# Kernel optimization log

Measured on AMD Instinct MI355X. Metric: run time of the kernel, lower is better.

Reference implementation:

```python
import jax, jax.numpy as jnp
import numpy as np

RANK = 4
IN_FEATURES = 1024
OUT_FEATURES = 1024
ALPHA = 1.0
SCALING = ALPHA / RANK


def setup_inputs() -> dict:
    key = jax.random.key(0)
    kx, ka = jax.random.split(key)
    x = jax.random.normal(kx, (4, 8192, IN_FEATURES), dtype=jnp.float32)
    # kaiming_uniform_(a=sqrt(5)) on [rank, in_features]: bound = sqrt(3) * gain / sqrt(fan_in)
    # gain = sqrt(2/(1+a^2)) = sqrt(1/3); fan_in = in_features -> bound = 1/sqrt(in_features)
    bound = 1.0 / np.sqrt(IN_FEATURES)
    lora_A = jax.random.uniform(ka, (RANK, IN_FEATURES), dtype=jnp.float32, minval=-bound, maxval=bound)
    # original init is zeros for B; use random values so the output/gradients are non-trivial
    lora_B = jax.random.normal(jax.random.fold_in(key, 7), (OUT_FEATURES, RANK), dtype=jnp.float32) * 0.02
    return {"x": x, "lora_A": lora_A, "lora_B": lora_B}


def reference(x, lora_A, lora_B):
    # h = scaling * (x @ A^T) @ B^T   (dropout p=0 -> identity)
    h = jnp.einsum('bsi,ri->bsr', x, lora_A)      # [B, S, rank]
    h = jnp.einsum('bsr,or->bso', h, lora_B)      # [B, S, out_features]
    return h * SCALING
```

## Files before the change

kernel.cpp:

```cpp
#include <hip/hip_runtime.h>
#include <stdint.h>

#define IN_F 1024
#define OUT_F 1024
#define SCALING 0.25f
#define TILE_ROWS 16
#define BLOCK 256

__global__ __launch_bounds__(BLOCK, 3) void lora_tile(
    const float* __restrict__ x, const float* __restrict__ A,
    const float* __restrict__ B, float* __restrict__ out, int nrows) {
  __shared__ float4 hf[TILE_ROWS];

  const int t = threadIdx.x;
  const int lane = t & 63;
  const int wave = t >> 6;
  const int row0 = blockIdx.x * TILE_ROWS;
  if (row0 >= nrows) return;

  const float4* __restrict__ x4 =
      (const float4*)(x + (size_t)(row0 + wave * 4) * IN_F);
  const float4* __restrict__ A4 = (const float4*)A;

  float4 xr[4][4];
#pragma unroll
  for (int i = 0; i < 4; ++i)
#pragma unroll
    for (int k = 0; k < 4; ++k) xr[i][k] = x4[i * 256 + lane + 64 * k];

  float4 a[4][4];
#pragma unroll
  for (int k = 0; k < 4; ++k)
#pragma unroll
    for (int r = 0; r < 4; ++r) a[r][k] = A4[r * 256 + lane + 64 * k];

  float p[4][4];
#pragma unroll
  for (int i = 0; i < 4; ++i)
#pragma unroll
    for (int r = 0; r < 4; ++r) p[i][r] = 0.f;

#pragma unroll
  for (int i = 0; i < 4; ++i)
#pragma unroll
    for (int k = 0; k < 4; ++k) {
      const float4 xv = xr[i][k];
#pragma unroll
      for (int r = 0; r < 4; ++r)
        p[i][r] += xv.x * a[r][k].x + xv.y * a[r][k].y + xv.z * a[r][k].z +
                   xv.w * a[r][k].w;
    }

  const float4* __restrict__ B4 = (const float4*)B;
  const float4 bf0 = B4[4 * t + 0];
  const float4 bf1 = B4[4 * t + 1];
  const float4 bf2 = B4[4 * t + 2];
  const float4 bf3 = B4[4 * t + 3];

#pragma unroll
  for (int off = 1; off < 64; off <<= 1)
#pragma unroll
    for (int i = 0; i < 4; ++i)
#pragma unroll
      for (int r = 0; r < 4; ++r) p[i][r] += __shfl_xor(p[i][r], off, 64);

  if (lane == 0) {
#pragma unroll
    for (int i = 0; i < 4; ++i)
      hf[wave * 4 + i] =
          make_float4(p[i][0] * SCALING, p[i][1] * SCALING, p[i][2] * SCALING,
                      p[i][3] * SCALING);
  }
  __syncthreads();

  float4* __restrict__ out4 = (float4*)out;
#pragma unroll
  for (int r = 0; r < TILE_ROWS; ++r) {
    const float4 h = hf[r];
    float4 res;
    res.x = h.x * bf0.x + h.y * bf0.y + h.z * bf0.z + h.w * bf0.w;
    res.y = h.x * bf1.x + h.y * bf1.y + h.z * bf1.z + h.w * bf1.w;
    res.z = h.x * bf2.x + h.y * bf2.y + h.z * bf2.z + h.w * bf2.w;
    res.w = h.x * bf3.x + h.y * bf3.y + h.z * bf3.z + h.w * bf3.w;
    out4[(size_t)(row0 + r) * (OUT_F / 4) + t] = res;
  }
}

extern "C" void kernel_launch(void* const* d_in, const int* in_sizes, int n_in,
                              void* d_out, int out_size, void* d_ws,
                              size_t ws_size, hipStream_t stream) {
  const float* x = (const float*)d_in[0];
  const float* A = (const float*)d_in[1];
  const float* B = (const float*)d_in[2];
  float* out = (float*)d_out;

  const int nrows = in_sizes[0] / IN_F;
  const int blocks = (nrows + TILE_ROWS - 1) / TILE_ROWS;
  lora_tile<<<blocks, BLOCK, 0, stream>>>(x, A, B, out, nrows);
}
```

Measured before the change: 232.7 us.

## Use persistent waves with register-resident A/B and double-buffered row streaming

Replaces the one-block-per-16-rows grid with a fixed persistent grid of 512 blocks. Each wave loops over 16-row groups, keeping A and B in registers and double-buffering x loads two rows at a time so the next loads overlap the current compute and stores. Each wave handles its own rows end to end, with no shared memory or block barrier. This cuts per-block launch and reload overhead and the sync, but raises register pressure (occupancy hint lowered to 2) and serialises each wave's rows.

```diff
diff --git a/kernel.cpp b/kernel.cpp
--- a/kernel.cpp
+++ b/kernel.cpp
@@ -4,85 +4,134 @@
 #define IN_F 1024
 #define OUT_F 1024
 #define SCALING 0.25f
-#define TILE_ROWS 16
 #define BLOCK 256
+#define NBLOCKS 512
+#define NITER 8
 
-__global__ __launch_bounds__(BLOCK, 3) void lora_tile(
+__global__ __launch_bounds__(BLOCK, 2) void lora_stream(
     const float* __restrict__ x, const float* __restrict__ A,
     const float* __restrict__ B, float* __restrict__ out, int nrows) {
-  __shared__ float4 hf[TILE_ROWS];
+  const int lane = threadIdx.x & 63;
+  const int gwave = (int)((blockIdx.x * BLOCK + threadIdx.x) >> 6);
+  const int nwaves = (int)(gridDim.x * (BLOCK / 64));
 
-  const int t = threadIdx.x;
-  const int lane = t & 63;
-  const int wave = t >> 6;
-  const int row0 = blockIdx.x * TILE_ROWS;
-  if (row0 >= nrows) return;
-
-  const float4* __restrict__ x4 =
-      (const float4*)(x + (size_t)(row0 + wave * 4) * IN_F);
   const float4* __restrict__ A4 = (const float4*)A;
-
-  float4 xr[4][4];
-#pragma unroll
-  for (int i = 0; i < 4; ++i)
-#pragma unroll
-    for (int k = 0; k < 4; ++k) xr[i][k] = x4[i * 256 + lane + 64 * k];
+  const float4* __restrict__ B4 = (const float4*)B;
+  const float4* __restrict__ X4 = (const float4*)x;
+  float4* __restrict__ out4 = (float4*)out;
 
   float4 a[4][4];
 #pragma unroll
+  for (int r = 0; r < 4; ++r)
+#pragma unroll
+    for (int k = 0; k < 4; ++k) a[r][k] = A4[r * 256 + lane + 64 * k];
+
+  float4 b[4][4];
+#pragma unroll
   for (int k = 0; k < 4; ++k)
 #pragma unroll
-    for (int r = 0; r < 4; ++r) a[r][k] = A4[r * 256 + lane + 64 * k];
+    for (int c = 0; c < 4; ++c) b[k][c] = B4[4 * (lane + 64 * k) + c];
 
-  float p[4][4];
+  for (int grp = gwave; grp * 16 < nrows; grp += nwaves) {
+    const int base = grp * 16;
+    if (base + 16 <= nrows) {
+      float4 xr[2][8];
 #pragma unroll
-  for (int i = 0; i < 4; ++i)
+      for (int j = 0; j < 2; ++j)
 #pragma unroll
-    for (int r = 0; r < 4; ++r) p[i][r] = 0.f;
+        for (int k = 0; k < 4; ++k)
+          xr[0][j * 4 + k] = X4[(size_t)(base + j) * 256 + lane + 64 * k];
 
 #pragma unroll
-  for (int i = 0; i < 4; ++i)
+      for (int it = 0; it < NITER; ++it) {
+        if (it + 1 < NITER) {
 #pragma unroll
-    for (int k = 0; k < 4; ++k) {
-      const float4 xv = xr[i][k];
+          for (int j = 0; j < 2; ++j)
 #pragma unroll
-      for (int r = 0; r < 4; ++r)
-        p[i][r] += xv.x * a[r][k].x + xv.y * a[r][k].y + xv.z * a[r][k].z +
-                   xv.w * a[r][k].w;
-    }
+            for (int k = 0; k < 4; ++k)
+              xr[(it + 1) & 1][j * 4 + k] =
+                  X4[(size_t)(base + 2 * (it + 1) + j) * 256 + lane + 64 * k];
+        }
 
-  const float4* __restrict__ B4 = (const float4*)B;
-  const float4 bf0 = B4[4 * t + 0];
-  const float4 bf1 = B4[4 * t + 1];
-  const float4 bf2 = B4[4 * t + 2];
-  const float4 bf3 = B4[4 * t + 3];
+        float p[2][4];
+#pragma unroll
+        for (int j = 0; j < 2; ++j)
+#pragma unroll
+          for (int r = 0; r < 4; ++r) p[j][r] = 0.f;
 
 #pragma unroll
-  for (int off = 1; off < 64; off <<= 1)
+        for (int j = 0; j < 2; ++j)
 #pragma unroll
-    for (int i = 0; i < 4; ++i)
+          for (int k = 0; k < 4; ++k) {
+            const float4 xv = xr[it & 1][j * 4 + k];
 #pragma unroll
-      for (int r = 0; r < 4; ++r) p[i][r] += __shfl_xor(p[i][r], off, 64);
+            for (int r = 0; r < 4; ++r)
+              p[j][r] += xv.x * a[r][k].x + xv.y * a[r][k].y +
+                         xv.z * a[r][k].z + xv.w * a[r][k].w;
+          }
 
-  if (lane == 0) {
 #pragma unroll
-    for (int i = 0; i < 4; ++i)
-      hf[wave * 4 + i] =
-          make_float4(p[i][0] * SCALING, p[i][1] * SCALING, p[i][2] * SCALING,
-                      p[i][3] * SCALING);
-  }
-  __syncthreads();
+        for (int off = 1; off < 64; off <<= 1)
+#pragma unroll
+          for (int j = 0; j < 2; ++j)
+#pragma unroll
+            for (int r = 0; r < 4; ++r)
+              p[j][r] += __shfl_xor(p[j][r], off, 64);
 
-  float4* __restrict__ out4 = (float4*)out;
 #pragma unroll
-  for (int r = 0; r < TILE_ROWS; ++r) {
-    const float4 h = hf[r];
-    float4 res;
-    res.x = h.x * bf0.x + h.y * bf0.y + h.z * bf0.z + h.w * bf0.w;
-    res.y = h.x * bf1.x + h.y * bf1.y + h.z * bf1.z + h.w * bf1.w;
-    res.z = h.x * bf2.x + h.y * bf2.y + h.z * bf2.z + h.w * bf2.w;
-    res.w = h.x * bf3.x + h.y * bf3.y + h.z * bf3.z + h.w * bf3.w;
-    out4[(size_t)(row0 + r) * (OUT_F / 4) + t] = res;
+        for (int j = 0; j < 2; ++j) {
+          const float h0 = p[j][0] * SCALING;
+          const float h1 = p[j][1] * SCALING;
+          const float h2 = p[j][2] * SCALING;
+          const float h3 = p[j][3] * SCALING;
+          const size_t orow = (size_t)(base + 2 * it + j) * 256;
+#pragma unroll
+          for (int k = 0; k < 4; ++k) {
+            float4 res;
+            res.x = h0 * b[k][0].x + h1 * b[k][0].y + h2 * b[k][0].z +
+                    h3 * b[k][0].w;
+            res.y = h0 * b[k][1].x + h1 * b[k][1].y + h2 * b[k][1].z +
+                    h3 * b[k][1].w;
+            res.z = h0 * b[k][2].x + h1 * b[k][2].y + h2 * b[k][2].z +
+                    h3 * b[k][2].w;
+            res.w = h0 * b[k][3].x + h1 * b[k][3].y + h2 * b[k][3].z +
+                    h3 * b[k][3].w;
+            out4[orow + lane + 64 * k] = res;
+          }
+        }
+      }
+    } else {
+      for (int row = base; row < nrows; ++row) {
+        float q[4] = {0.f, 0.f, 0.f, 0.f};
+#pragma unroll
+        for (int k = 0; k < 4; ++k) {
+          const float4 xv = X4[(size_t)row * 256 + lane + 64 * k];
+#pragma unroll
+          for (int r = 0; r < 4; ++r)
+            q[r] += xv.x * a[r][k].x + xv.y * a[r][k].y + xv.z * a[r][k].z +
+                    xv.w * a[r][k].w;
+        }
+#pragma unroll
+        for (int off = 1; off < 64; off <<= 1)
+#pragma unroll
+          for (int r = 0; r < 4; ++r) q[r] += __shfl_xor(q[r], off, 64);
+        const float h0 = q[0] * SCALING, h1 = q[1] * SCALING,
+                    h2 = q[2] * SCALING, h3 = q[3] * SCALING;
+#pragma unroll
+        for (int k = 0; k < 4; ++k) {
+          float4 res;
+          res.x = h0 * b[k][0].x + h1 * b[k][0].y + h2 * b[k][0].z +
+                  h3 * b[k][0].w;
+          res.y = h0 * b[k][1].x + h1 * b[k][1].y + h2 * b[k][1].z +
+                  h3 * b[k][1].w;
+          res.z = h0 * b[k][2].x + h1 * b[k][2].y + h2 * b[k][2].z +
+                  h3 * b[k][2].w;
+          res.w = h0 * b[k][3].x + h1 * b[k][3].y + h2 * b[k][3].z +
+                  h3 * b[k][3].w;
+          out4[(size_t)row * 256 + lane + 64 * k] = res;
+        }
+      }
+    }
   }
 }
 
@@ -95,6 +144,5 @@
   float* out = (float*)d_out;
 
   const int nrows = in_sizes[0] / IN_F;
-  const int blocks = (nrows + TILE_ROWS - 1) / TILE_ROWS;
-  lora_tile<<<blocks, BLOCK, 0, stream>>>(x, A, B, out, nrows);
+  lora_stream<<<NBLOCKS, BLOCK, 0, stream>>>(x, A, B, out, nrows);
 }
```

After: 245.2 us. 5.4% more time.
